# Kernel optimization log

Measured on AMD Instinct MI355X. Metric: run time of the kernel, lower is better.

## Reference

```python
import jax, jax.numpy as jnp
import numpy as np

D_MODEL = 1024
H = 16
D_K = D_MODEL // H


def setup_inputs() -> dict:
    key = jax.random.key(0)
    ks = jax.random.split(key, 11)
    B, S = 2, 2048
    scale = 1.0 / np.sqrt(D_MODEL)
    inp = {
        "q": jax.random.normal(ks[0], (B, S, D_MODEL), jnp.float32),
        "k": jax.random.normal(ks[1], (B, S, D_MODEL), jnp.float32),
        "v": jax.random.normal(ks[2], (B, S, D_MODEL), jnp.float32),
        "w_q": jax.random.normal(ks[3], (D_MODEL, D_MODEL), jnp.float32) * scale,
        "b_q": jnp.zeros((D_MODEL,), jnp.float32),
        "w_k": jax.random.normal(ks[4], (D_MODEL, D_MODEL), jnp.float32) * scale,
        "b_k": jnp.zeros((D_MODEL,), jnp.float32),
        "w_v": jax.random.normal(ks[5], (D_MODEL, D_MODEL), jnp.float32) * scale,
        "b_v": jnp.zeros((D_MODEL,), jnp.float32),
        "w_o": jax.random.normal(ks[6], (D_MODEL, D_MODEL), jnp.float32) * scale,
        "b_o": jnp.zeros((D_MODEL,), jnp.float32),
    }
    return inp


def reference(q, k, v, w_q, b_q, w_k, b_k, w_v, b_v, w_o, b_o):
    B, S, _ = q.shape
    # QKV projections (nn.Linear: x @ W^T + b)
    query = q @ w_q.T + b_q
    key_ = k @ w_k.T + b_k
    value = v @ w_v.T + b_v
    # [B, S, H, D_K] -> [B, H, S, D_K]
    query = query.reshape(B, S, H, D_K).transpose(0, 2, 1, 3)
    key_ = key_.reshape(B, S, H, D_K).transpose(0, 2, 1, 3)
    value = value.reshape(B, S, H, D_K).transpose(0, 2, 1, 3)
    # scores: [B, H, S, S]
    scores = jnp.einsum("bhqd,bhkd->bhqk", query, key_) / jnp.sqrt(
        jnp.asarray(D_K, query.dtype)
    )
    attn = jax.nn.softmax(scores, axis=-1)
    # dropout rate is 0.0 -> identity
    x = jnp.einsum("bhqk,bhkd->bhqd", attn, value)  # [B, H, S, D_K]
    x = x.transpose(0, 2, 1, 3).reshape(B, S, D_MODEL)
    return x @ w_o.T + b_o
```

## Files before the change

### kernel.cpp

```cpp
#include <hip/hip_runtime.h>
#include <hip/hip_bf16.h>


typedef __attribute__((ext_vector_type(8))) short short8;
typedef __attribute__((ext_vector_type(4))) float f32x4;

__device__ __forceinline__ unsigned short f2b(float f) {
  union { float f; unsigned u; } x; x.f = f;
  unsigned r = (x.u + 0x7FFFu + ((x.u >> 16) & 1u)) >> 16;
  return (unsigned short)r;
}

__device__ __forceinline__ int swz7(int row) { return ((row ^ (row >> 3)) & 7) << 4; }

__device__ __forceinline__ void gload16(const void* g, void* l) {
  __builtin_amdgcn_global_load_lds((const __attribute__((address_space(1))) void*)g,
                                   (__attribute__((address_space(3))) void*)l, 16, 0, 0);
}

__global__ __launch_bounds__(256) void cvt_bf16(const float* __restrict__ s,
                                                unsigned short* __restrict__ d, int n) {
  int i = (blockIdx.x * 256 + threadIdx.x) * 8;
  if (i >= n) return;
  float4 a = *(const float4*)(s + i);
  float4 b = *(const float4*)(s + i + 4);
  short8 o;
  o[0] = (short)f2b(a.x); o[1] = (short)f2b(a.y); o[2] = (short)f2b(a.z); o[3] = (short)f2b(a.w);
  o[4] = (short)f2b(b.x); o[5] = (short)f2b(b.y); o[6] = (short)f2b(b.z); o[7] = (short)f2b(b.w);
  *(short8*)(d + i) = o;
}

template <int MODE>
__global__ __launch_bounds__(256, 2) void gemm_bt(const unsigned short* __restrict__ A,
                                                  const unsigned short* __restrict__ W,
                                                  const float* __restrict__ bias,
                                                  void* __restrict__ Out) {
  constexpr int K = 1024;
  const int m0 = blockIdx.y * 128, n0 = blockIdx.x * 128;
  __shared__ __align__(16) unsigned short At[128 * 64];
  __shared__ __align__(16) unsigned short Bt[128 * 64];
  const int t = threadIdx.x;
  const int w = t >> 6, l = t & 63;
  const int wr = w >> 1, wc = w & 1;
  const int lr = l & 15, hi = l >> 4;
  f32x4 acc[4][4] = {};
  for (int kt = 0; kt < 16; ++kt) {
    __syncthreads();
#pragma unroll
    for (int i = 0; i < 4; ++i) {
      int c = i * 256 + t;
      int row = c >> 3, cb = (c & 7) * 16;
      const char* src = (const char*)(A + (size_t)(m0 + row) * K + kt * 64);
      gload16(src + (cb ^ swz7(row)), At + c * 8);
    }
#pragma unroll
    for (int i = 0; i < 4; ++i) {
      int c = i * 256 + t;
      int row = c >> 3, cb = (c & 7) * 16;
      const char* src = (const char*)(W + (size_t)(n0 + row) * K + kt * 64);
      gload16(src + (cb ^ swz7(row)), Bt + c * 8);
    }
    __syncthreads();
#pragma unroll
    for (int ks = 0; ks < 2; ++ks) {
      short8 af[4], bf[4];
#pragma unroll
      for (int mt = 0; mt < 4; ++mt) {
        int row = wr * 64 + mt * 16 + lr;
        af[mt] = *(const short8*)((const char*)At + row * 128 + ((ks * 64 + hi * 16) ^ swz7(row)));
      }
#pragma unroll
      for (int nt = 0; nt < 4; ++nt) {
        int row = wc * 64 + nt * 16 + lr;
        bf[nt] = *(const short8*)((const char*)Bt + row * 128 + ((ks * 64 + hi * 16) ^ swz7(row)));
      }
#pragma unroll
      for (int mt = 0; mt < 4; ++mt)
#pragma unroll
        for (int nt = 0; nt < 4; ++nt)
          acc[mt][nt] = __builtin_amdgcn_mfma_f32_16x16x32_bf16(af[mt], bf[nt], acc[mt][nt], 0, 0, 0);
    }
  }
#pragma unroll
  for (int nt = 0; nt < 4; ++nt) {
    int n = n0 + wc * 64 + nt * 16 + lr;
    float bn = bias[n];
#pragma unroll
    for (int mt = 0; mt < 4; ++mt) {
#pragma unroll
      for (int r = 0; r < 4; ++r) {
        int m = m0 + wr * 64 + mt * 16 + hi * 4 + r;
        float v = acc[mt][nt][r] + bn;
        if (MODE == 0) {
          size_t dst = ((size_t)((m >> 11) * 16 + (n >> 6))) * (2048 * 64) +
                       (size_t)(m & 2047) * 64 + (n & 63);
          ((unsigned short*)Out)[dst] = f2b(v);
        } else {
          ((float*)Out)[(size_t)m * 1024 + n] = v;
        }
      }
    }
  }
}

__global__ __launch_bounds__(256, 2) void attn_fwd(const unsigned short* __restrict__ Q,
                                                   const unsigned short* __restrict__ Kh,
                                                   const unsigned short* __restrict__ Vh,
                                                   unsigned short* __restrict__ Oout) {
  const int bh = blockIdx.x >> 5, qt = blockIdx.x & 31;
  const int t = threadIdx.x, w = t >> 6, l = t & 63;
  const int lr = l & 15, hi = l >> 4;
  __shared__ __align__(16) unsigned short Kl[64 * 64];
  __shared__ __align__(16) unsigned short Vt[64 * 64];
  __shared__ __align__(16) unsigned short Pl[4][16 * 64];
  const unsigned short* Qb = Q + (size_t)bh * 2048 * 64;
  const unsigned short* Kb = Kh + (size_t)bh * 2048 * 64;
  const unsigned short* Vb = Vh + (size_t)bh * 2048 * 64;
  short8 qf[2];
#pragma unroll
  for (int ks = 0; ks < 2; ++ks)
    qf[ks] = *(const short8*)(Qb + (size_t)(qt * 64 + w * 16 + lr) * 64 + ks * 32 + hi * 8);
  f32x4 oacc[4] = {};
  float mrow[4], lrow[4];
#pragma unroll
  for (int r = 0; r < 4; ++r) { mrow[r] = -1e30f; lrow[r] = 0.f; }

  for (int kt = 0; kt < 32; ++kt) {
    __syncthreads();
#pragma unroll
    for (int i = 0; i < 2; ++i) {
      int c = i * 256 + t;
      int row = c >> 3, cb = (c & 7) * 16;
      const char* src = (const char*)(Kb + (size_t)(kt * 64 + row) * 64);
      gload16(src + (cb ^ swz7(row)), Kl + c * 8);
    }
#pragma unroll
    for (int i = 0; i < 2; ++i) {
      int c = i * 256 + t;
      int row = c >> 3, d0 = (c & 7) * 8;
      short8 v8 = *(const short8*)(Vb + (size_t)(kt * 64 + row) * 64 + d0);
#pragma unroll
      for (int j = 0; j < 8; ++j) {
        int dd = d0 + j;
        *(unsigned short*)((char*)Vt + dd * 128 + ((row * 2) ^ swz7(dd))) = (unsigned short)v8[j];
      }
    }
    __syncthreads();
    f32x4 sacc[4] = {};
#pragma unroll
    for (int nt = 0; nt < 4; ++nt) {
#pragma unroll
      for (int ks = 0; ks < 2; ++ks) {
        int row = nt * 16 + lr;
        short8 bfr = *(const short8*)((const char*)Kl + row * 128 + ((ks * 64 + hi * 16) ^ swz7(row)));
        sacc[nt] = __builtin_amdgcn_mfma_f32_16x16x32_bf16(qf[ks], bfr, sacc[nt], 0, 0, 0);
      }
    }
#pragma unroll
    for (int r = 0; r < 4; ++r) {
      float mx = fmaxf(fmaxf(sacc[0][r], sacc[1][r]), fmaxf(sacc[2][r], sacc[3][r]));
#pragma unroll
      for (int d = 1; d < 16; d <<= 1) mx = fmaxf(mx, __shfl_xor(mx, d, 64));
      float mnew = fmaxf(mrow[r], mx * 0.125f);
      float sc = __expf(mrow[r] - mnew);
#pragma unroll
      for (int dt = 0; dt < 4; ++dt) oacc[dt][r] *= sc;
      float rsum = 0.f;
      unsigned short pb[4];
#pragma unroll
      for (int nt = 0; nt < 4; ++nt) {
        float p = __expf(sacc[nt][r] * 0.125f - mnew);
        rsum += p;
        pb[nt] = f2b(p);
      }
#pragma unroll
      for (int d = 1; d < 16; d <<= 1) rsum += __shfl_xor(rsum, d, 64);
      lrow[r] = lrow[r] * sc + rsum;
      mrow[r] = mnew;
      int prow = hi * 4 + r;
#pragma unroll
      for (int nt = 0; nt < 4; ++nt)
        *(unsigned short*)((char*)Pl[w] + prow * 128 + (((nt * 16 + lr) * 2) ^ swz7(prow))) = pb[nt];
    }
    short8 paf[2];
#pragma unroll
    for (int ks = 0; ks < 2; ++ks)
      paf[ks] = *(const short8*)((const char*)Pl[w] + lr * 128 + ((ks * 64 + hi * 16) ^ swz7(lr)));
#pragma unroll
    for (int dt = 0; dt < 4; ++dt) {
#pragma unroll
      for (int ks = 0; ks < 2; ++ks) {
        int vrow = dt * 16 + lr;
        short8 bfr = *(const short8*)((const char*)Vt + vrow * 128 + ((ks * 64 + hi * 16) ^ swz7(vrow)));
        oacc[dt] = __builtin_amdgcn_mfma_f32_16x16x32_bf16(paf[ks], bfr, oacc[dt], 0, 0, 0);
      }
    }
  }
#pragma unroll
  for (int r = 0; r < 4; ++r) {
    float inv = 1.f / lrow[r];
    int s = qt * 64 + w * 16 + hi * 4 + r;
    size_t base = ((size_t)(bh >> 4) * 2048 + s) * 1024 + (size_t)(bh & 15) * 64;
#pragma unroll
    for (int dt = 0; dt < 4; ++dt) Oout[base + dt * 16 + lr] = f2b(oacc[dt][r] * inv);
  }
}

extern "C" void kernel_launch(void* const* d_in, const int* in_sizes, int n_in,
                              void* d_out, int out_size, void* d_ws, size_t ws_size,
                              hipStream_t stream) {
  const float* q   = (const float*)d_in[0];
  const float* k   = (const float*)d_in[1];
  const float* v   = (const float*)d_in[2];
  const float* w_q = (const float*)d_in[3];
  const float* b_q = (const float*)d_in[4];
  const float* w_k = (const float*)d_in[5];
  const float* b_k = (const float*)d_in[6];
  const float* w_v = (const float*)d_in[7];
  const float* b_v = (const float*)d_in[8];
  const float* w_o = (const float*)d_in[9];
  const float* b_o = (const float*)d_in[10];

  unsigned short* ws = (unsigned short*)d_ws;
  const size_t M1 = 1024 * 1024;
  unsigned short* qb = ws;
  unsigned short* kb = ws + 4 * M1;
  unsigned short* vb = ws + 8 * M1;
  unsigned short* wq = ws + 12 * M1;
  unsigned short* wk = ws + 13 * M1;
  unsigned short* wv = ws + 14 * M1;
  unsigned short* wo = ws + 15 * M1;
  unsigned short* Qh = ws + 16 * M1;
  unsigned short* Kh = ws + 20 * M1;
  unsigned short* Vh = ws + 24 * M1;
  unsigned short* Ah = ws + 28 * M1;

  cvt_bf16<<<2048, 256, 0, stream>>>(q, qb, 4194304);
  cvt_bf16<<<2048, 256, 0, stream>>>(k, kb, 4194304);
  cvt_bf16<<<2048, 256, 0, stream>>>(v, vb, 4194304);
  cvt_bf16<<<512, 256, 0, stream>>>(w_q, wq, 1048576);
  cvt_bf16<<<512, 256, 0, stream>>>(w_k, wk, 1048576);
  cvt_bf16<<<512, 256, 0, stream>>>(w_v, wv, 1048576);
  cvt_bf16<<<512, 256, 0, stream>>>(w_o, wo, 1048576);

  dim3 g(8, 32);
  gemm_bt<0><<<g, 256, 0, stream>>>(qb, wq, b_q, Qh);
  gemm_bt<0><<<g, 256, 0, stream>>>(kb, wk, b_k, Kh);
  gemm_bt<0><<<g, 256, 0, stream>>>(vb, wv, b_v, Vh);

  attn_fwd<<<1024, 256, 0, stream>>>(Qh, Kh, Vh, Ah);

  gemm_bt<1><<<g, 256, 0, stream>>>(Ah, wo, b_o, d_out);
}
```

Baseline: 346.3 us.

## Batch QKV GEMMs, split-KV attention with merge, pre-transposed V, narrower output GEMM tiles

```diff
diff --git a/kernel.cpp b/kernel.cpp
--- a/kernel.cpp
+++ b/kernel.cpp
@@ -3,6 +3,7 @@
 
 
 typedef __attribute__((ext_vector_type(8))) short short8;
+typedef __attribute__((ext_vector_type(4))) short short4_t;
 typedef __attribute__((ext_vector_type(4))) float f32x4;
 
 __device__ __forceinline__ unsigned short f2b(float f) {
@@ -30,20 +31,29 @@
   *(short8*)(d + i) = o;
 }
 
-template <int MODE>
-__global__ __launch_bounds__(256, 2) void gemm_bt(const unsigned short* __restrict__ A,
-                                                  const unsigned short* __restrict__ W,
-                                                  const float* __restrict__ bias,
-                                                  void* __restrict__ Out) {
+template <int BN, int MODE>
+__global__ __launch_bounds__(256, 2) void gemm_t(
+    const unsigned short* __restrict__ A0, const unsigned short* __restrict__ A1,
+    const unsigned short* __restrict__ A2, const unsigned short* __restrict__ Wt,
+    const float* __restrict__ b0, const float* __restrict__ b1, const float* __restrict__ b2,
+    void* __restrict__ O0, void* __restrict__ O1, void* __restrict__ O2) {
   constexpr int K = 1024;
-  const int m0 = blockIdx.y * 128, n0 = blockIdx.x * 128;
+  constexpr int NT = BN / 32;
+  const int m0 = blockIdx.y * 128, n0 = blockIdx.x * BN;
+  const int chunk = (MODE == 3) ? (n0 >> 10) : 0;
+  const unsigned short* A = A0;
+  const float* bias = b0;
+  if (MODE == 3) {
+    A = chunk == 0 ? A0 : chunk == 1 ? A1 : A2;
+    bias = chunk == 0 ? b0 : chunk == 1 ? b1 : b2;
+  }
   __shared__ __align__(16) unsigned short At[128 * 64];
-  __shared__ __align__(16) unsigned short Bt[128 * 64];
+  __shared__ __align__(16) unsigned short Bt[BN * 64];
   const int t = threadIdx.x;
   const int w = t >> 6, l = t & 63;
   const int wr = w >> 1, wc = w & 1;
   const int lr = l & 15, hi = l >> 4;
-  f32x4 acc[4][4] = {};
+  f32x4 acc[4][NT] = {};
   for (int kt = 0; kt < 16; ++kt) {
     __syncthreads();
 #pragma unroll
@@ -54,50 +64,80 @@
       gload16(src + (cb ^ swz7(row)), At + c * 8);
     }
 #pragma unroll
-    for (int i = 0; i < 4; ++i) {
+    for (int i = 0; i < BN / 32; ++i) {
       int c = i * 256 + t;
       int row = c >> 3, cb = (c & 7) * 16;
-      const char* src = (const char*)(W + (size_t)(n0 + row) * K + kt * 64);
+      const char* src = (const char*)(Wt + (size_t)(n0 + row) * K + kt * 64);
       gload16(src + (cb ^ swz7(row)), Bt + c * 8);
     }
     __syncthreads();
 #pragma unroll
     for (int ks = 0; ks < 2; ++ks) {
-      short8 af[4], bf[4];
+      short8 af[4], bf[NT];
 #pragma unroll
       for (int mt = 0; mt < 4; ++mt) {
         int row = wr * 64 + mt * 16 + lr;
         af[mt] = *(const short8*)((const char*)At + row * 128 + ((ks * 64 + hi * 16) ^ swz7(row)));
       }
 #pragma unroll
-      for (int nt = 0; nt < 4; ++nt) {
-        int row = wc * 64 + nt * 16 + lr;
+      for (int nt = 0; nt < NT; ++nt) {
+        int row = wc * (BN / 2) + nt * 16 + lr;
         bf[nt] = *(const short8*)((const char*)Bt + row * 128 + ((ks * 64 + hi * 16) ^ swz7(row)));
       }
 #pragma unroll
       for (int mt = 0; mt < 4; ++mt)
 #pragma unroll
-        for (int nt = 0; nt < 4; ++nt)
+        for (int nt = 0; nt < NT; ++nt)
           acc[mt][nt] = __builtin_amdgcn_mfma_f32_16x16x32_bf16(af[mt], bf[nt], acc[mt][nt], 0, 0, 0);
     }
   }
-#pragma unroll
-  for (int nt = 0; nt < 4; ++nt) {
-    int n = n0 + wc * 64 + nt * 16 + lr;
-    float bn = bias[n];
-#pragma unroll
-    for (int mt = 0; mt < 4; ++mt) {
-#pragma unroll
-      for (int r = 0; r < 4; ++r) {
-        int m = m0 + wr * 64 + mt * 16 + hi * 4 + r;
-        float v = acc[mt][nt][r] + bn;
-        if (MODE == 0) {
+  if (MODE == 1) {
+    float* O = (float*)O0;
+#pragma unroll
+    for (int nt = 0; nt < NT; ++nt) {
+      int n = n0 + wc * (BN / 2) + nt * 16 + lr;
+      float bn = bias[n];
+#pragma unroll
+      for (int mt = 0; mt < 4; ++mt)
+#pragma unroll
+        for (int r = 0; r < 4; ++r) {
+          int m = m0 + wr * 64 + mt * 16 + hi * 4 + r;
+          O[(size_t)m * 1024 + n] = acc[mt][nt][r] + bn;
+        }
+    }
+  } else if (chunk <= 1) {
+    unsigned short* O = (unsigned short*)(chunk ? O1 : O0);
+    const float sc = (chunk == 0) ? 0.125f : 1.0f;
+#pragma unroll
+    for (int nt = 0; nt < NT; ++nt) {
+      int n = (n0 + wc * (BN / 2) + nt * 16 + lr) & 1023;
+      float bn = bias[n];
+#pragma unroll
+      for (int mt = 0; mt < 4; ++mt)
+#pragma unroll
+        for (int r = 0; r < 4; ++r) {
+          int m = m0 + wr * 64 + mt * 16 + hi * 4 + r;
+          float v = (acc[mt][nt][r] + bn) * sc;
           size_t dst = ((size_t)((m >> 11) * 16 + (n >> 6))) * (2048 * 64) +
                        (size_t)(m & 2047) * 64 + (n & 63);
-          ((unsigned short*)Out)[dst] = f2b(v);
-        } else {
-          ((float*)Out)[(size_t)m * 1024 + n] = v;
+          O[dst] = f2b(v);
         }
+    }
+  } else {
+    unsigned short* O = (unsigned short*)O2;
+#pragma unroll
+    for (int nt = 0; nt < NT; ++nt) {
+      int n = (n0 + wc * (BN / 2) + nt * 16 + lr) & 1023;
+      float bn = bias[n];
+#pragma unroll
+      for (int mt = 0; mt < 4; ++mt) {
+        int mb = m0 + wr * 64 + mt * 16 + hi * 4;
+        short4_t pk;
+#pragma unroll
+        for (int r = 0; r < 4; ++r) pk[r] = (short)f2b(acc[mt][nt][r] + bn);
+        size_t dst = ((size_t)((mb >> 11) * 16 + (n >> 6))) * (64 * 2048) +
+                     (size_t)(n & 63) * 2048 + (mb & 2047);
+        *(short4_t*)(O + dst) = pk;
       }
     }
   }
@@ -105,17 +145,19 @@
 
 __global__ __launch_bounds__(256, 2) void attn_fwd(const unsigned short* __restrict__ Q,
                                                    const unsigned short* __restrict__ Kh,
-                                                   const unsigned short* __restrict__ Vh,
-                                                   unsigned short* __restrict__ Oout) {
-  const int bh = blockIdx.x >> 5, qt = blockIdx.x & 31;
+                                                   const unsigned short* __restrict__ Vtg,
+                                                   float* __restrict__ Op,
+                                                   float* __restrict__ ml) {
+  const int bid = blockIdx.x;
+  const int qt = bid & 31, bh = (bid >> 5) & 31, hf = bid >> 10;
   const int t = threadIdx.x, w = t >> 6, l = t & 63;
   const int lr = l & 15, hi = l >> 4;
   __shared__ __align__(16) unsigned short Kl[64 * 64];
-  __shared__ __align__(16) unsigned short Vt[64 * 64];
+  __shared__ __align__(16) unsigned short Vl[64 * 64];
   __shared__ __align__(16) unsigned short Pl[4][16 * 64];
-  const unsigned short* Qb = Q + (size_t)bh * 2048 * 64;
-  const unsigned short* Kb = Kh + (size_t)bh * 2048 * 64;
-  const unsigned short* Vb = Vh + (size_t)bh * 2048 * 64;
+  const unsigned short* Qb = Q + (size_t)bh * 131072;
+  const unsigned short* Kb = Kh + (size_t)bh * 131072 + (size_t)hf * 65536;
+  const unsigned short* Vb = Vtg + (size_t)bh * 131072 + (size_t)hf * 1024;
   short8 qf[2];
 #pragma unroll
   for (int ks = 0; ks < 2; ++ks)
@@ -125,7 +167,7 @@
 #pragma unroll
   for (int r = 0; r < 4; ++r) { mrow[r] = -1e30f; lrow[r] = 0.f; }
 
-  for (int kt = 0; kt < 32; ++kt) {
+  for (int kt = 0; kt < 16; ++kt) {
     __syncthreads();
 #pragma unroll
     for (int i = 0; i < 2; ++i) {
@@ -137,13 +179,9 @@
 #pragma unroll
     for (int i = 0; i < 2; ++i) {
       int c = i * 256 + t;
-      int row = c >> 3, d0 = (c & 7) * 8;
-      short8 v8 = *(const short8*)(Vb + (size_t)(kt * 64 + row) * 64 + d0);
-#pragma unroll
-      for (int j = 0; j < 8; ++j) {
-        int dd = d0 + j;
-        *(unsigned short*)((char*)Vt + dd * 128 + ((row * 2) ^ swz7(dd))) = (unsigned short)v8[j];
-      }
+      int row = c >> 3, cb = (c & 7) * 16;
+      const char* src = (const char*)(Vb + (size_t)row * 2048 + kt * 64);
+      gload16(src + (cb ^ swz7(row)), Vl + c * 8);
     }
     __syncthreads();
     f32x4 sacc[4] = {};
@@ -161,7 +199,7 @@
       float mx = fmaxf(fmaxf(sacc[0][r], sacc[1][r]), fmaxf(sacc[2][r], sacc[3][r]));
 #pragma unroll
       for (int d = 1; d < 16; d <<= 1) mx = fmaxf(mx, __shfl_xor(mx, d, 64));
-      float mnew = fmaxf(mrow[r], mx * 0.125f);
+      float mnew = fmaxf(mrow[r], mx);
       float sc = __expf(mrow[r] - mnew);
 #pragma unroll
       for (int dt = 0; dt < 4; ++dt) oacc[dt][r] *= sc;
@@ -169,7 +207,7 @@
       unsigned short pb[4];
 #pragma unroll
       for (int nt = 0; nt < 4; ++nt) {
-        float p = __expf(sacc[nt][r] * 0.125f - mnew);
+        float p = __expf(sacc[nt][r] - mnew);
         rsum += p;
         pb[nt] = f2b(p);
       }
@@ -191,19 +229,49 @@
 #pragma unroll
       for (int ks = 0; ks < 2; ++ks) {
         int vrow = dt * 16 + lr;
-        short8 bfr = *(const short8*)((const char*)Vt + vrow * 128 + ((ks * 64 + hi * 16) ^ swz7(vrow)));
+        short8 bfr = *(const short8*)((const char*)Vl + vrow * 128 + ((ks * 64 + hi * 16) ^ swz7(vrow)));
         oacc[dt] = __builtin_amdgcn_mfma_f32_16x16x32_bf16(paf[ks], bfr, oacc[dt], 0, 0, 0);
       }
     }
   }
+  const size_t ro = ((size_t)hf * 32 + bh) * 2048 + qt * 64 + w * 16;
 #pragma unroll
   for (int r = 0; r < 4; ++r) {
-    float inv = 1.f / lrow[r];
-    int s = qt * 64 + w * 16 + hi * 4 + r;
-    size_t base = ((size_t)(bh >> 4) * 2048 + s) * 1024 + (size_t)(bh & 15) * 64;
-#pragma unroll
-    for (int dt = 0; dt < 4; ++dt) Oout[base + dt * 16 + lr] = f2b(oacc[dt][r] * inv);
-  }
+    int sl = hi * 4 + r;
+#pragma unroll
+    for (int dt = 0; dt < 4; ++dt)
+      Op[(ro + sl) * 64 + dt * 16 + lr] = oacc[dt][r];
+    if (lr == 0) {
+      ml[(ro + sl) * 2] = mrow[r];
+      ml[(ro + sl) * 2 + 1] = lrow[r];
+    }
+  }
+}
+
+__global__ __launch_bounds__(256) void merge_halves(const float* __restrict__ Op,
+                                                    const float* __restrict__ ml,
+                                                    unsigned short* __restrict__ Ah) {
+  const int t = threadIdx.x;
+  const int row = blockIdx.x * 32 + (t >> 3);
+  const int d0 = (t & 7) * 8;
+  const float ma = ml[(size_t)row * 2], la = ml[(size_t)row * 2 + 1];
+  const float mb = ml[(size_t)(65536 + row) * 2], lb = ml[(size_t)(65536 + row) * 2 + 1];
+  const float m = fmaxf(ma, mb);
+  const float ea = __expf(ma - m), eb = __expf(mb - m);
+  const float inv = 1.f / (la * ea + lb * eb);
+  const float ca = ea * inv, cb = eb * inv;
+  const float* o1 = Op + (size_t)row * 64 + d0;
+  const float* o2 = o1 + (size_t)65536 * 64;
+  float4 a0 = *(const float4*)o1, a1 = *(const float4*)(o1 + 4);
+  float4 b0 = *(const float4*)o2, b1 = *(const float4*)(o2 + 4);
+  short8 pk;
+  pk[0] = (short)f2b(a0.x * ca + b0.x * cb); pk[1] = (short)f2b(a0.y * ca + b0.y * cb);
+  pk[2] = (short)f2b(a0.z * ca + b0.z * cb); pk[3] = (short)f2b(a0.w * ca + b0.w * cb);
+  pk[4] = (short)f2b(a1.x * ca + b1.x * cb); pk[5] = (short)f2b(a1.y * ca + b1.y * cb);
+  pk[6] = (short)f2b(a1.z * ca + b1.z * cb); pk[7] = (short)f2b(a1.w * ca + b1.w * cb);
+  const int bh = row >> 11, s = row & 2047;
+  size_t dst = ((size_t)(bh >> 4) * 2048 + s) * 1024 + (size_t)(bh & 15) * 64 + d0;
+  *(short8*)(Ah + dst) = pk;
 }
 
 extern "C" void kernel_launch(void* const* d_in, const int* in_sizes, int n_in,
@@ -222,33 +290,33 @@
   const float* b_o = (const float*)d_in[10];
 
   unsigned short* ws = (unsigned short*)d_ws;
-  const size_t M1 = 1024 * 1024;
-  unsigned short* qb = ws;
-  unsigned short* kb = ws + 4 * M1;
-  unsigned short* vb = ws + 8 * M1;
-  unsigned short* wq = ws + 12 * M1;
-  unsigned short* wk = ws + 13 * M1;
-  unsigned short* wv = ws + 14 * M1;
-  unsigned short* wo = ws + 15 * M1;
-  unsigned short* Qh = ws + 16 * M1;
-  unsigned short* Kh = ws + 20 * M1;
-  unsigned short* Vh = ws + 24 * M1;
-  unsigned short* Ah = ws + 28 * M1;
+  const size_t M1 = 1u << 20;
+  unsigned short* qb   = ws;
+  unsigned short* kb   = ws + 4 * M1;
+  unsigned short* vb   = ws + 8 * M1;
+  unsigned short* wcat = ws + 12 * M1;
+  unsigned short* wo   = ws + 16 * M1;
+  unsigned short* Qh   = ws + 17 * M1;
+  unsigned short* Kh   = ws + 21 * M1;
+  unsigned short* Vtg  = ws + 25 * M1;
+  float*          mlp  = (float*)(ws + 29 * M1);
+  float*          Op   = (float*)ws;
+  unsigned short* Ah   = ws + 21 * M1;
 
   cvt_bf16<<<2048, 256, 0, stream>>>(q, qb, 4194304);
   cvt_bf16<<<2048, 256, 0, stream>>>(k, kb, 4194304);
   cvt_bf16<<<2048, 256, 0, stream>>>(v, vb, 4194304);
-  cvt_bf16<<<512, 256, 0, stream>>>(w_q, wq, 1048576);
-  cvt_bf16<<<512, 256, 0, stream>>>(w_k, wk, 1048576);
-  cvt_bf16<<<512, 256, 0, stream>>>(w_v, wv, 1048576);
+  cvt_bf16<<<512, 256, 0, stream>>>(w_q, wcat, 1048576);
+  cvt_bf16<<<512, 256, 0, stream>>>(w_k, wcat + M1, 1048576);
+  cvt_bf16<<<512, 256, 0, stream>>>(w_v, wcat + 2 * M1, 1048576);
   cvt_bf16<<<512, 256, 0, stream>>>(w_o, wo, 1048576);
 
-  dim3 g(8, 32);
-  gemm_bt<0><<<g, 256, 0, stream>>>(qb, wq, b_q, Qh);
-  gemm_bt<0><<<g, 256, 0, stream>>>(kb, wk, b_k, Kh);
-  gemm_bt<0><<<g, 256, 0, stream>>>(vb, wv, b_v, Vh);
-
-  attn_fwd<<<1024, 256, 0, stream>>>(Qh, Kh, Vh, Ah);
-
-  gemm_bt<1><<<g, 256, 0, stream>>>(Ah, wo, b_o, d_out);
-}
+  gemm_t<128, 3><<<dim3(24, 32), 256, 0, stream>>>(qb, kb, vb, wcat, b_q, b_k, b_v,
+                                                   Qh, Kh, Vtg);
+
+  attn_fwd<<<2048, 256, 0, stream>>>(Qh, Kh, Vtg, Op, mlp);
+  merge_halves<<<2048, 256, 0, stream>>>(Op, mlp, Ah);
+
+  gemm_t<64, 1><<<dim3(16, 32), 256, 0, stream>>>(Ah, nullptr, nullptr, wo, b_o,
+                                                  nullptr, nullptr, d_out, nullptr, nullptr);
+}
```

After: 304.7 us. -12.0%, faster.
